# Performance work log

Measured on AMD Instinct MI355X. Metric: run time of the kernel, lower is better.

Reference implementation:

```python
import jax, jax.numpy as jnp
import numpy as np

N_EMBD = 1024
N_HEAD = 16
LATENT = 64
HEAD_DIM = N_EMBD // N_HEAD
B, T = 2, 2048
SCALE = 1.0 / np.sqrt(LATENT)


def setup_inputs() -> dict:
    key = jax.random.key(0)
    ks = jax.random.split(key, 10)
    s = lambda fan_in: 1.0 / np.sqrt(fan_in)
    return {
        "x": jax.random.normal(ks[0], (B, T, N_EMBD), dtype=jnp.float32),
        "Wq": jax.random.normal(ks[1], (N_EMBD, N_EMBD), dtype=jnp.float32) * s(N_EMBD),
        "bq": jnp.zeros((N_EMBD,), dtype=jnp.float32),
        "Wk": jax.random.normal(ks[2], (N_EMBD, N_HEAD * LATENT), dtype=jnp.float32) * s(N_EMBD),
        "bk": jnp.zeros((N_HEAD * LATENT,), dtype=jnp.float32),
        "Wv": jax.random.normal(ks[3], (N_EMBD, N_HEAD * LATENT), dtype=jnp.float32) * s(N_EMBD),
        "bv": jnp.zeros((N_HEAD * LATENT,), dtype=jnp.float32),
        "Wo": jax.random.normal(ks[4], (N_HEAD * LATENT, N_EMBD), dtype=jnp.float32) * s(N_HEAD * LATENT),
        "bo": jnp.zeros((N_EMBD,), dtype=jnp.float32),
        "Wc": jax.random.normal(ks[5], (HEAD_DIM, LATENT), dtype=jnp.float32) * s(HEAD_DIM),
    }


def reference(x, Wq, bq, Wk, bk, Wv, bv, Wo, bo, Wc):
    Bv, Tv, C = x.shape
    # projections
    q = (x @ Wq + bq).reshape(Bv, Tv, N_HEAD, HEAD_DIM)        # [B,T,H,Dh]
    k = (x @ Wk + bk).reshape(Bv, Tv, N_HEAD, LATENT)          # [B,T,H,L]
    v = (x @ Wv + bv).reshape(Bv, Tv, N_HEAD, LATENT)          # [B,T,H,L]
    # compress q into latent dim: [B,T,H,L]
    qc = jnp.einsum("bthd,dl->bthl", q, Wc)
    # attention scores [B,H,T,T]
    att = jnp.einsum("bthl,bshl->bhts", qc, k) * SCALE
    causal = jnp.tril(jnp.ones((Tv, Tv), dtype=bool))
    att = jnp.where(causal[None, None], att, -jnp.inf)
    att = jax.nn.softmax(att, axis=-1)
    y = jnp.einsum("bhts,bshl->bthl", att, v).reshape(Bv, Tv, N_HEAD * LATENT)
    return y @ Wo + bo
```

## Files before the change

### kernel.cpp

```cpp
#include <hip/hip_runtime.h>
#include <stdint.h>

#define TT 2048
#define BB 2
#define MROWS (BB*TT)
#define LSCALE 0.18033688011112043f

typedef unsigned short u16;
typedef __bf16 bf16x8 __attribute__((ext_vector_type(8)));
typedef float f32x4 __attribute__((ext_vector_type(4)));
typedef short s16x8 __attribute__((ext_vector_type(8)));
typedef unsigned short u16x4 __attribute__((ext_vector_type(4)));

#define GLOBAL_AS const __attribute__((address_space(1))) void*
#define LDS_AS __attribute__((address_space(3))) void*

__device__ __forceinline__ u16 f2b(float f){
  uint32_t u = __builtin_bit_cast(uint32_t, f);
  u = (u + 0x7FFFu + ((u >> 16) & 1u)) >> 16;
  return (u16)u;
}
__device__ __forceinline__ float b2f(u16 u){
  return __builtin_bit_cast(float, (uint32_t)u << 16);
}

__global__ void cvt_bf16(const float* __restrict__ in, u16* __restrict__ out, int n4){
  int i = blockIdx.x * 256 + threadIdx.x;
  if (i < n4){
    float4 v = ((const float4*)in)[i];
    u16x4 o; o.x = f2b(v.x); o.y = f2b(v.y); o.z = f2b(v.z); o.w = f2b(v.w);
    ((u16x4*)out)[i] = o;
  }
}

__global__ __launch_bounds__(256) void build_wqc(const float* __restrict__ Wq,
                                                 const float* __restrict__ Wc,
                                                 const float* __restrict__ bq,
                                                 float* __restrict__ Wqc,
                                                 float* __restrict__ bqc){
  __shared__ float wc[4096];
  const int t = threadIdx.x;
  #pragma unroll
  for (int i = 0; i < 16; ++i) wc[i * 256 + t] = Wc[i * 256 + t];
  __syncthreads();
  if (blockIdx.x == 256){
    #pragma unroll
    for (int i = 0; i < 4; ++i){
      int nn = t * 4 + i;
      int h = nn >> 6, lc = nn & 63;
      float acc = 0.f;
      #pragma unroll
      for (int dd = 0; dd < 64; ++dd) acc += bq[h * 64 + dd] * wc[dd * 64 + lc];
      bqc[nn] = acc;
    }
    return;
  }
  const int idx = blockIdx.x * 256 + t;
  const int d = idx >> 6;
  const int h = (idx >> 2) & 15;
  const int lq = idx & 3;
  float wqr[64];
  const float4* wq4 = (const float4*)(Wq + (size_t)d * 1024 + h * 64);
  #pragma unroll
  for (int i = 0; i < 16; ++i){
    float4 v = wq4[i];
    wqr[i * 4 + 0] = v.x; wqr[i * 4 + 1] = v.y; wqr[i * 4 + 2] = v.z; wqr[i * 4 + 3] = v.w;
  }
  float* outp = Wqc + (size_t)d * 1024 + h * 64 + lq * 16;
  #pragma unroll
  for (int j = 0; j < 16; ++j){
    int lc = lq * 16 + j;
    float acc = 0.f;
    #pragma unroll
    for (int dd = 0; dd < 64; ++dd) acc += wqr[dd] * wc[dd * 64 + lc];
    outp[j] = acc;
  }
}

__global__ void transpose_w4(const float* __restrict__ s0, const float* __restrict__ s1,
                             const float* __restrict__ s2, const float* __restrict__ s3,
                             u16* __restrict__ o0, u16* __restrict__ o1,
                             u16* __restrict__ o2, u16* __restrict__ o3){
  const int z = blockIdx.z;
  const float* in = (z == 0) ? s0 : (z == 1) ? s1 : (z == 2) ? s2 : s3;
  u16* out = (z == 0) ? o0 : (z == 1) ? o1 : (z == 2) ? o2 : o3;
  __shared__ float t[32][33];
  int tx = threadIdx.x & 31, ty = threadIdx.x >> 5;
  int c0 = blockIdx.x * 32, r0 = blockIdx.y * 32;
  #pragma unroll
  for (int i = 0; i < 32; i += 8)
    t[ty + i][tx] = in[(size_t)(r0 + ty + i) * 1024 + c0 + tx];
  __syncthreads();
  #pragma unroll
  for (int i = 0; i < 32; i += 8)
    out[(size_t)(c0 + ty + i) * 1024 + r0 + tx] = f2b(t[tx][ty + i]);
}

__global__ void transpose_v(const u16* __restrict__ vb, u16* __restrict__ vt){
  __shared__ u16 t[32][34];
  int tx = threadIdx.x & 31, ty = threadIdx.x >> 5;
  int s0 = blockIdx.x * 32, d0 = blockIdx.y * 32, bh = blockIdx.z;
  int b = bh >> 4, h = bh & 15;
  #pragma unroll
  for (int i = 0; i < 32; i += 8)
    t[ty + i][tx] = vb[(size_t)(b * TT + s0 + ty + i) * 1024 + h * 64 + d0 + tx];
  __syncthreads();
  #pragma unroll
  for (int i = 0; i < 32; i += 8)
    vt[((size_t)bh * 64 + d0 + ty + i) * TT + s0 + tx] = t[tx][ty + i];
}

__device__ __forceinline__ void gemm_tile(const u16* __restrict__ A, const u16* __restrict__ BT,
                                          int m0, int n0, int K, f32x4 (&acc)[4][4],
                                          u16* As, u16* Bs, int tid){
  const int wv = tid >> 6, l = tid & 63;
  const int aoff = ((wv >> 1) * 64 + (l & 15)) * 32 + ((l >> 4) << 3);
  const int boff = ((wv & 1) * 64 + (l & 15)) * 32 + ((l >> 4) << 3);
  const int ob0 = wv * 1024 + l * 16;
  for (int kt = 0; kt < K; kt += 32){
    __syncthreads();
    #pragma unroll
    for (int j = 0; j < 2; ++j){
      int ob = ob0 + j * 4096;
      int row = ob >> 6, col = (ob & 63) >> 1;
      __builtin_amdgcn_global_load_lds((GLOBAL_AS)(A + (size_t)(m0 + row) * 1024 + kt + col),
                                       (LDS_AS)(As + wv * 512 + j * 2048), 16, 0, 0);
      __builtin_amdgcn_global_load_lds((GLOBAL_AS)(BT + (size_t)(n0 + row) * 1024 + kt + col),
                                       (LDS_AS)(Bs + wv * 512 + j * 2048), 16, 0, 0);
    }
    __syncthreads();
    bf16x8 av[4], bw[4];
    #pragma unroll
    for (int m = 0; m < 4; ++m) av[m] = *(const bf16x8*)(As + aoff + m * 512);
    #pragma unroll
    for (int n = 0; n < 4; ++n) bw[n] = *(const bf16x8*)(Bs + boff + n * 512);
    #pragma unroll
    for (int m = 0; m < 4; ++m)
      #pragma unroll
      for (int n = 0; n < 4; ++n)
        acc[m][n] = __builtin_amdgcn_mfma_f32_16x16x32_bf16(av[m], bw[n], acc[m][n], 0, 0, 0);
  }
}

__global__ __launch_bounds__(256) void gemm_qkv(
    const u16* __restrict__ xb,
    const u16* __restrict__ W0T, const u16* __restrict__ W1T, const u16* __restrict__ W2T,
    const float* __restrict__ b0, const float* __restrict__ b1, const float* __restrict__ b2,
    u16* __restrict__ o0, u16* __restrict__ o1, u16* __restrict__ o2){
  __shared__ u16 As[4096], Bs[4096];
  const int z = blockIdx.z;
  const u16* BT = (z == 0) ? W0T : (z == 1) ? W1T : W2T;
  const float* bias = (z == 0) ? b0 : (z == 1) ? b1 : b2;
  u16* Out = (z == 0) ? o0 : (z == 1) ? o1 : o2;
  const float osc = (z == 0) ? LSCALE : 1.0f;
  const int n0 = blockIdx.x * 128, m0 = blockIdx.y * 128;
  const int tid = threadIdx.x, wv = tid >> 6, l = tid & 63;
  f32x4 acc[4][4] = {};
  gemm_tile(xb, BT, m0, n0, 1024, acc, As, Bs, tid);
  const int wr = wv >> 1, wc = wv & 1;
  #pragma unroll
  for (int n = 0; n < 4; ++n){
    int col = n0 + wc * 64 + n * 16 + (l & 15);
    float bb = bias[col];
    #pragma unroll
    for (int m = 0; m < 4; ++m){
      int r0 = m0 + wr * 64 + m * 16 + ((l >> 4) << 2);
      #pragma unroll
      for (int r = 0; r < 4; ++r)
        Out[(size_t)(r0 + r) * 1024 + col] = f2b((acc[m][n][r] + bb) * osc);
    }
  }
}

__global__ __launch_bounds__(256) void gemm_fp32out(
    const u16* __restrict__ A, const u16* __restrict__ BT,
    const float* __restrict__ bias, float* __restrict__ Out){
  __shared__ u16 As[4096], Bs[4096];
  const int n0 = blockIdx.x * 128, m0 = blockIdx.y * 128;
  const int tid = threadIdx.x, wv = tid >> 6, l = tid & 63;
  f32x4 acc[4][4] = {};
  gemm_tile(A, BT, m0, n0, 1024, acc, As, Bs, tid);
  const int wr = wv >> 1, wc = wv & 1;
  #pragma unroll
  for (int n = 0; n < 4; ++n){
    int col = n0 + wc * 64 + n * 16 + (l & 15);
    float bb = bias[col];
    #pragma unroll
    for (int m = 0; m < 4; ++m){
      int r0 = m0 + wr * 64 + m * 16 + ((l >> 4) << 2);
      #pragma unroll
      for (int r = 0; r < 4; ++r)
        Out[(size_t)(r0 + r) * 1024 + col] = acc[m][n][r] + bb;
    }
  }
}

__device__ const uint8_t gtab[48] = {
  31, 95, 30, 143,  94, 29, 93, 28, 142,  92, 27, 91, 26, 141,
  90, 25, 89, 24, 140,  88, 23, 87, 22, 139,  86, 21, 85, 20, 138,
  84, 19, 83, 18, 137,  82, 17, 81, 16, 136,  80, 135, 134, 133, 132,
  131, 130, 129, 128
};

__global__ __launch_bounds__(256) void attn(
    const u16* __restrict__ qcg, const u16* __restrict__ kg,
    const u16* __restrict__ vtg, u16* __restrict__ yg,
    u16* __restrict__ yp, float* __restrict__ mp, float* __restrict__ lp){
  __shared__ u16 Ks[4096], Vs[4096];
  __shared__ u16 Ps[4096];
  const int idx = blockIdx.x;
  const int g = idx >> 5, bh = idx & 31;
  const int gv_ = gtab[g];
  const int qt = gv_ & 31, piece = gv_ >> 6;
  const int hh = (qt + 2) >> 1;
  const int st0 = (piece == 1) ? hh : 0;
  const int st1 = (piece == 0) ? hh : qt + 1;
  const int pid = (piece == 2) ? -1 : ((31 - qt) * 32 + bh) * 2 + piece;
  const int b = bh >> 4, h = bh & 15;
  const int q0 = qt * 64;
  const int tid = threadIdx.x, wv = tid >> 6, l = tid & 63;
  const int c4 = l >> 4, q16 = l & 15;
  const size_t base = (size_t)b * TT * 1024 + h * 64;
  const u16* Q = qcg + base;
  const u16* K = kg + base;
  const u16* Vt = vtg + (size_t)bh * 64 * TT;

  const int sr = tid >> 3;
  const int sc = (tid & 7) ^ (sr & 7);
  const u16* gK = K + (size_t)sr * 1024 + sc * 8;
  const u16* gV = Vt + (size_t)sr * TT + sc * 8;

  bf16x8 qf[2];
  {
    int qr = q0 + wv * 16 + q16;
    #pragma unroll
    for (int ks = 0; ks < 2; ++ks)
      qf[ks] = *(const bf16x8*)(Q + (size_t)qr * 1024 + ks * 32 + (c4 << 3));
  }
  f32x4 yacc[4] = {};
  float mrow = -1e30f, srow = 0.f;

  uint32_t* const PsW = (uint32_t*)Ps + wv * 512 + q16 * 32;
  const int pm = (q16 & 7) << 2;

  u16* const kd = Ks + wv * 512;
  u16* const vd = Vs + wv * 512;

  for (int st = st0; st < st1; ++st){
    {
      const size_t o = (size_t)st * 64;
      __builtin_amdgcn_global_load_lds((GLOBAL_AS)(gK + o * 1024), (LDS_AS)kd, 16, 0, 0);
      __builtin_amdgcn_global_load_lds((GLOBAL_AS)(gK + (o + 32) * 1024), (LDS_AS)(kd + 2048), 16, 0, 0);
      __builtin_amdgcn_global_load_lds((GLOBAL_AS)(gV + o), (LDS_AS)vd, 16, 0, 0);
      __builtin_amdgcn_global_load_lds((GLOBAL_AS)(gV + o + 32 * TT), (LDS_AS)(vd + 2048), 16, 0, 0);
    }
    asm volatile("s_waitcnt vmcnt(0)" ::: "memory");
    __builtin_amdgcn_sched_barrier(0);
    __builtin_amdgcn_s_barrier();
    __builtin_amdgcn_sched_barrier(0);
    const int s0 = st * 64;
    f32x4 sf[4] = {};
    __builtin_amdgcn_s_setprio(1);
    #pragma unroll
    for (int ks = 0; ks < 2; ++ks)
      #pragma unroll
      for (int nf = 0; nf < 4; ++nf){
        int r = nf * 16 + q16, c = ks * 4 + c4;
        bf16x8 kf = *(const bf16x8*)(Ks + (r * 8 + (c ^ (r & 7))) * 8);
        sf[nf] = __builtin_amdgcn_mfma_f32_16x16x32_bf16(kf, qf[ks], sf[nf], 0, 0, 0);
      }
    __builtin_amdgcn_s_setprio(0);
    const int qa = q0 + wv * 16 + q16;
    float p[4][4];
    const bool domask = (st == qt);
    #pragma unroll
    for (int nf = 0; nf < 4; ++nf)
      #pragma unroll
      for (int r = 0; r < 4; ++r){
        float v_ = sf[nf][r];
        if (domask && (s0 + nf * 16 + c4 * 4 + r > qa)) v_ = -1e30f;
        p[nf][r] = v_;
      }
    float tmax = p[0][0];
    #pragma unroll
    for (int nf = 0; nf < 4; ++nf)
      #pragma unroll
      for (int r = 0; r < 4; ++r) tmax = fmaxf(tmax, p[nf][r]);
    tmax = fmaxf(tmax, __shfl_xor(tmax, 16));
    tmax = fmaxf(tmax, __shfl_xor(tmax, 32));
    if (__any(tmax > mrow + 8.0f)){
      float mnew = fmaxf(mrow, tmax);
      float resc = exp2f(mrow - mnew);
      srow *= resc;
      mrow = mnew;
      #pragma unroll
      for (int df = 0; df < 4; ++df)
        #pragma unroll
        for (int r = 0; r < 4; ++r) yacc[df][r] *= resc;
    }
    float tsum = 0.f;
    #pragma unroll
    for (int nf = 0; nf < 4; ++nf)
      #pragma unroll
      for (int r = 0; r < 4; ++r){ float e = exp2f(p[nf][r] - mrow); p[nf][r] = e; tsum += e; }
    tsum += __shfl_xor(tsum, 16);
    tsum += __shfl_xor(tsum, 32);
    srow += tsum;
    #pragma unroll
    for (int nf = 0; nf < 4; ++nf){
      uint32_t w0, w1;
      asm volatile("v_cvt_pk_bf16_f32 %0, %1, %2" : "=v"(w0) : "v"(p[nf][0]), "v"(p[nf][1]));
      asm volatile("v_cvt_pk_bf16_f32 %0, %1, %2" : "=v"(w1) : "v"(p[nf][2]), "v"(p[nf][3]));
      *(uint64_t*)(PsW + ((nf * 8 + c4 * 2) ^ pm)) = (uint64_t)w0 | ((uint64_t)w1 << 32);
    }
    asm volatile("s_waitcnt lgkmcnt(0)" ::: "memory");
    __builtin_amdgcn_sched_barrier(0);
    __builtin_amdgcn_s_setprio(1);
    #pragma unroll
    for (int ks2 = 0; ks2 < 2; ++ks2){
      bf16x8 pf = *(const bf16x8*)(PsW + ((ks2 * 16 + c4 * 4) ^ pm));
      #pragma unroll
      for (int df = 0; df < 4; ++df){
        int rd = df * 16 + q16, cd = ks2 * 4 + c4;
        bf16x8 vf = *(const bf16x8*)(Vs + (rd * 8 + (cd ^ (rd & 7))) * 8);
        yacc[df] = __builtin_amdgcn_mfma_f32_16x16x32_bf16(vf, pf, yacc[df], 0, 0, 0);
      }
    }
    __builtin_amdgcn_s_setprio(0);
    __builtin_amdgcn_s_barrier();
  }

  if (pid >= 0){
    const int qq = wv * 16 + q16;
    #pragma unroll
    for (int df = 0; df < 4; ++df){
      int d0 = df * 16 + c4 * 4;
      #pragma unroll
      for (int r = 0; r < 4; ++r)
        yp[(size_t)pid * 4096 + qq * 64 + d0 + r] = f2b(yacc[df][r]);
    }
    if (c4 == 0){
      mp[pid * 64 + qq] = mrow;
      lp[pid * 64 + qq] = srow;
    }
  } else {
    const float inv = 1.f / srow;
    const int qq = q0 + wv * 16 + q16;
    #pragma unroll
    for (int df = 0; df < 4; ++df){
      int d0 = df * 16 + c4 * 4;
      #pragma unroll
      for (int r = 0; r < 4; ++r)
        yg[(size_t)(b * TT + qq) * 1024 + h * 64 + d0 + r] = f2b(yacc[df][r] * inv);
    }
  }
}

__global__ __launch_bounds__(256) void attn_combine(
    const u16* __restrict__ yp, const float* __restrict__ mp, const float* __restrict__ lp,
    u16* __restrict__ yg){
  const int cid = blockIdx.x;
  const int qt = 31 - (cid >> 5), bh = cid & 31;
  const int pid0 = cid * 2;
  const int t = threadIdx.x;
  const int q = t >> 2, dc = (t & 3) * 16;
  float m1 = mp[pid0 * 64 + q], m2 = mp[(pid0 + 1) * 64 + q];
  float l1 = lp[pid0 * 64 + q], l2 = lp[(pid0 + 1) * 64 + q];
  float ms = fmaxf(m1, m2);
  float w1 = exp2f(m1 - ms), w2 = exp2f(m2 - ms);
  float inv = 1.f / (l1 * w1 + l2 * w2);
  w1 *= inv; w2 *= inv;
  const int b = bh >> 4, h = bh & 15;
  const s16x8* p1 = (const s16x8*)(yp + (size_t)pid0 * 4096 + q * 64 + dc);
  const s16x8* p2 = (const s16x8*)(yp + (size_t)(pid0 + 1) * 4096 + q * 64 + dc);
  u16* dst = yg + (size_t)(b * TT + qt * 64 + q) * 1024 + h * 64 + dc;
  #pragma unroll
  for (int j2 = 0; j2 < 2; ++j2){
    s16x8 a = p1[j2], c = p2[j2];
    s16x8 o;
    #pragma unroll
    for (int j = 0; j < 8; ++j)
      o[j] = (short)f2b(b2f((u16)a[j]) * w1 + b2f((u16)c[j]) * w2);
    *(s16x8*)(dst + j2 * 8) = o;
  }
}

extern "C" void kernel_launch(void* const* d_in, const int* in_sizes, int n_in,
                              void* d_out, int out_size, void* d_ws, size_t ws_size,
                              hipStream_t stream){
  (void)in_sizes; (void)n_in; (void)out_size; (void)ws_size;
  const float* x  = (const float*)d_in[0];
  const float* Wq = (const float*)d_in[1];
  const float* bq = (const float*)d_in[2];
  const float* Wk = (const float*)d_in[3];
  const float* bk = (const float*)d_in[4];
  const float* Wv = (const float*)d_in[5];
  const float* bv = (const float*)d_in[6];
  const float* Wo = (const float*)d_in[7];
  const float* bo = (const float*)d_in[8];
  const float* Wc = (const float*)d_in[9];
  float* out = (float*)d_out;

  char* wsb = (char*)d_ws;
  u16* xb    = (u16*)(wsb);
  u16* yb    = (u16*)(wsb);
  u16* qcb   = (u16*)(wsb + (8u  << 20));
  u16* kb    = (u16*)(wsb + (16u << 20));
  u16* vb    = (u16*)(wsb + (24u << 20));
  u16* yp    = (u16*)(wsb + (24u << 20));
  u16* vtb   = (u16*)(wsb + (33u << 20));
  float* Wqcf = (float*)(wsb + (33u << 20));
  float* mp  = (float*)(wsb + (41u << 20));
  float* lp  = (float*)(wsb + (41u << 20) + (1u<<19));
  u16* WqcT  = (u16*)(wsb + (42u << 20));
  u16* WkT   = (u16*)(wsb + (44u << 20));
  u16* WvT   = (u16*)(wsb + (46u << 20));
  u16* WoT   = (u16*)(wsb + (48u << 20));
  float* bqc  = (float*)(wsb + (50u << 20));

  cvt_bf16<<<4096, 256, 0, stream>>>(x, xb, MROWS * 1024 / 4);
  build_wqc<<<257, 256, 0, stream>>>(Wq, Wc, bq, Wqcf, bqc);
  transpose_w4<<<dim3(32, 32, 4), 256, 0, stream>>>(Wqcf, Wk, Wv, Wo, WqcT, WkT, WvT, WoT);
  gemm_qkv<<<dim3(8, 32, 3), 256, 0, stream>>>(xb, WqcT, WkT, WvT, bqc, bk, bv, qcb, kb, vb);
  transpose_v<<<dim3(64, 2, 32), 256, 0, stream>>>(vb, vtb);
  attn<<<dim3(1536), 256, 0, stream>>>(qcb, kb, vtb, yb, yp, mp, lp);
  attn_combine<<<dim3(512), 256, 0, stream>>>(yp, mp, lp, yb);
  gemm_fp32out<<<dim3(8, 32), 256, 0, stream>>>(yb, WoT, bo, out);
}
```

Baseline: 132.0 us.

## Fuse prep kernels, write V transposed from QKV GEMM, shrink output GEMM tile

Merges the x conversion, Wq·Wc fold, and weight transposes into one prep launch, so the fp32 Wqc intermediate no longer makes a round trip through memory. The QKV GEMM now writes V directly in the transposed layout attention needs, which removes the separate transpose_v kernel. The output projection GEMM uses 64-row tiles, giving 512 blocks for better CU coverage. The risks are that the V epilogue's strided 2-byte stores are poorly coalesced and that one heterogeneous prep kernel may balance its work unevenly across blocks.

```diff
diff --git a/kernel.cpp b/kernel.cpp
--- a/kernel.cpp
+++ b/kernel.cpp
@@ -24,90 +24,83 @@
   return __builtin_bit_cast(float, (uint32_t)u << 16);
 }
 
-__global__ void cvt_bf16(const float* __restrict__ in, u16* __restrict__ out, int n4){
-  int i = blockIdx.x * 256 + threadIdx.x;
-  if (i < n4){
-    float4 v = ((const float4*)in)[i];
+__global__ __launch_bounds__(256) void prep(
+    const float* __restrict__ x, const float* __restrict__ Wq,
+    const float* __restrict__ Wc, const float* __restrict__ bq,
+    const float* __restrict__ Wk, const float* __restrict__ Wv,
+    const float* __restrict__ Wo,
+    u16* __restrict__ xb, u16* __restrict__ WqcT, u16* __restrict__ WkT,
+    u16* __restrict__ WvT, u16* __restrict__ WoT, float* __restrict__ bqc){
+  const int i = blockIdx.x, t = threadIdx.x;
+  if (i < 4096){
+    int id = i * 256 + t;
+    float4 v = ((const float4*)x)[id];
     u16x4 o; o.x = f2b(v.x); o.y = f2b(v.y); o.z = f2b(v.z); o.w = f2b(v.w);
-    ((u16x4*)out)[i] = o;
-  }
-}
-
-__global__ __launch_bounds__(256) void build_wqc(const float* __restrict__ Wq,
-                                                 const float* __restrict__ Wc,
-                                                 const float* __restrict__ bq,
-                                                 float* __restrict__ Wqc,
-                                                 float* __restrict__ bqc){
+    ((u16x4*)xb)[id] = o;
+    return;
+  }
+  if (i < 7168){
+    int j = i - 4096;
+    int z = j >> 10, rem = j & 1023;
+    const float* in = (z == 0) ? Wk : (z == 1) ? Wv : Wo;
+    u16* out = (z == 0) ? WkT : (z == 1) ? WvT : WoT;
+    __shared__ float tl[32][33];
+    int tx = t & 31, ty = t >> 5;
+    int c0 = (rem & 31) * 32, r0 = (rem >> 5) * 32;
+    #pragma unroll
+    for (int k = 0; k < 32; k += 8)
+      tl[ty + k][tx] = in[(size_t)(r0 + ty + k) * 1024 + c0 + tx];
+    __syncthreads();
+    #pragma unroll
+    for (int k = 0; k < 32; k += 8)
+      out[(size_t)(c0 + ty + k) * 1024 + r0 + tx] = f2b(tl[tx][ty + k]);
+    return;
+  }
   __shared__ float wc[4096];
-  const int t = threadIdx.x;
   #pragma unroll
-  for (int i = 0; i < 16; ++i) wc[i * 256 + t] = Wc[i * 256 + t];
+  for (int k = 0; k < 16; ++k) wc[k * 256 + t] = Wc[k * 256 + t];
   __syncthreads();
-  if (blockIdx.x == 256){
-    #pragma unroll
-    for (int i = 0; i < 4; ++i){
-      int nn = t * 4 + i;
+  if (i == 7424){
+    #pragma unroll
+    for (int k = 0; k < 4; ++k){
+      int nn = t * 4 + k;
       int h = nn >> 6, lc = nn & 63;
-      float acc = 0.f;
-      #pragma unroll
-      for (int dd = 0; dd < 64; ++dd) acc += bq[h * 64 + dd] * wc[dd * 64 + lc];
-      bqc[nn] = acc;
+      float a = 0.f;
+      #pragma unroll
+      for (int dd = 0; dd < 64; ++dd) a += bq[h * 64 + dd] * wc[dd * 64 + lc];
+      bqc[nn] = a;
     }
     return;
   }
-  const int idx = blockIdx.x * 256 + t;
-  const int d = idx >> 6;
-  const int h = (idx >> 2) & 15;
-  const int lq = idx & 3;
-  float wqr[64];
-  const float4* wq4 = (const float4*)(Wq + (size_t)d * 1024 + h * 64);
-  #pragma unroll
-  for (int i = 0; i < 16; ++i){
-    float4 v = wq4[i];
-    wqr[i * 4 + 0] = v.x; wqr[i * 4 + 1] = v.y; wqr[i * 4 + 2] = v.z; wqr[i * 4 + 3] = v.w;
-  }
-  float* outp = Wqc + (size_t)d * 1024 + h * 64 + lq * 16;
-  #pragma unroll
-  for (int j = 0; j < 16; ++j){
-    int lc = lq * 16 + j;
-    float acc = 0.f;
-    #pragma unroll
-    for (int dd = 0; dd < 64; ++dd) acc += wqr[dd] * wc[dd * 64 + lc];
-    outp[j] = acc;
-  }
-}
-
-__global__ void transpose_w4(const float* __restrict__ s0, const float* __restrict__ s1,
-                             const float* __restrict__ s2, const float* __restrict__ s3,
-                             u16* __restrict__ o0, u16* __restrict__ o1,
-                             u16* __restrict__ o2, u16* __restrict__ o3){
-  const int z = blockIdx.z;
-  const float* in = (z == 0) ? s0 : (z == 1) ? s1 : (z == 2) ? s2 : s3;
-  u16* out = (z == 0) ? o0 : (z == 1) ? o1 : (z == 2) ? o2 : o3;
-  __shared__ float t[32][33];
-  int tx = threadIdx.x & 31, ty = threadIdx.x >> 5;
-  int c0 = blockIdx.x * 32, r0 = blockIdx.y * 32;
-  #pragma unroll
-  for (int i = 0; i < 32; i += 8)
-    t[ty + i][tx] = in[(size_t)(r0 + ty + i) * 1024 + c0 + tx];
+  __shared__ float tile[64][65];
+  const int j = i - 7168;
+  const int db = j >> 4, hb = j & 15;
+  {
+    int dl = t >> 2, lq = t & 3;
+    const float4* wq4 = (const float4*)(Wq + (size_t)(db * 64 + dl) * 1024 + hb * 64);
+    float wqr[64];
+    #pragma unroll
+    for (int k = 0; k < 16; ++k){
+      float4 v = wq4[k];
+      wqr[k * 4] = v.x; wqr[k * 4 + 1] = v.y; wqr[k * 4 + 2] = v.z; wqr[k * 4 + 3] = v.w;
+    }
+    #pragma unroll
+    for (int jj = 0; jj < 16; ++jj){
+      int lc = lq * 16 + jj;
+      float a = 0.f;
+      #pragma unroll
+      for (int dd = 0; dd < 64; ++dd) a += wqr[dd] * wc[dd * 64 + lc];
+      tile[dl][lc] = a;
+    }
+  }
   __syncthreads();
-  #pragma unroll
-  for (int i = 0; i < 32; i += 8)
-    out[(size_t)(c0 + ty + i) * 1024 + r0 + tx] = f2b(t[tx][ty + i]);
-}
-
-__global__ void transpose_v(const u16* __restrict__ vb, u16* __restrict__ vt){
-  __shared__ u16 t[32][34];
-  int tx = threadIdx.x & 31, ty = threadIdx.x >> 5;
-  int s0 = blockIdx.x * 32, d0 = blockIdx.y * 32, bh = blockIdx.z;
-  int b = bh >> 4, h = bh & 15;
-  #pragma unroll
-  for (int i = 0; i < 32; i += 8)
-    t[ty + i][tx] = vb[(size_t)(b * TT + s0 + ty + i) * 1024 + h * 64 + d0 + tx];
-  __syncthreads();
-  #pragma unroll
-  for (int i = 0; i < 32; i += 8)
-    vt[((size_t)bh * 64 + d0 + ty + i) * TT + s0 + tx] = t[tx][ty + i];
+  {
+    int nl = t >> 2, dq = t & 3;
+    u16* dst = WqcT + (size_t)(hb * 64 + nl) * 1024 + db * 64 + dq * 16;
+    #pragma unroll
+    for (int k = 0; k < 16; ++k)
+      dst[k] = f2b(tile[dq * 16 + k][nl]);
+  }
 }
 
 __device__ __forceinline__ void gemm_tile(const u16* __restrict__ A, const u16* __restrict__ BT,
@@ -146,18 +139,36 @@
     const u16* __restrict__ xb,
     const u16* __restrict__ W0T, const u16* __restrict__ W1T, const u16* __restrict__ W2T,
     const float* __restrict__ b0, const float* __restrict__ b1, const float* __restrict__ b2,
-    u16* __restrict__ o0, u16* __restrict__ o1, u16* __restrict__ o2){
+    u16* __restrict__ o0, u16* __restrict__ o1, u16* __restrict__ vt){
   __shared__ u16 As[4096], Bs[4096];
   const int z = blockIdx.z;
   const u16* BT = (z == 0) ? W0T : (z == 1) ? W1T : W2T;
   const float* bias = (z == 0) ? b0 : (z == 1) ? b1 : b2;
-  u16* Out = (z == 0) ? o0 : (z == 1) ? o1 : o2;
-  const float osc = (z == 0) ? LSCALE : 1.0f;
   const int n0 = blockIdx.x * 128, m0 = blockIdx.y * 128;
   const int tid = threadIdx.x, wv = tid >> 6, l = tid & 63;
   f32x4 acc[4][4] = {};
   gemm_tile(xb, BT, m0, n0, 1024, acc, As, Bs, tid);
   const int wr = wv >> 1, wc = wv & 1;
+  if (z == 2){
+    const int bb_ = m0 >> 11;
+    #pragma unroll
+    for (int n = 0; n < 4; ++n){
+      int col = n0 + wc * 64 + n * 16 + (l & 15);
+      float bb = bias[col];
+      int h = col >> 6, d = col & 63;
+      u16* dcol = vt + ((size_t)(bb_ * 16 + h) * 64 + d) * TT;
+      #pragma unroll
+      for (int m = 0; m < 4; ++m){
+        int s = (m0 & 2047) + wr * 64 + m * 16 + ((l >> 4) << 2);
+        #pragma unroll
+        for (int r = 0; r < 4; ++r)
+          dcol[s + r] = f2b(acc[m][n][r] + bb);
+      }
+    }
+    return;
+  }
+  u16* Out = (z == 0) ? o0 : o1;
+  const float osc = (z == 0) ? LSCALE : 1.0f;
   #pragma unroll
   for (int n = 0; n < 4; ++n){
     int col = n0 + wc * 64 + n * 16 + (l & 15);
@@ -172,22 +183,49 @@
   }
 }
 
-__global__ __launch_bounds__(256) void gemm_fp32out(
+__global__ __launch_bounds__(256) void gemm_o(
     const u16* __restrict__ A, const u16* __restrict__ BT,
     const float* __restrict__ bias, float* __restrict__ Out){
-  __shared__ u16 As[4096], Bs[4096];
-  const int n0 = blockIdx.x * 128, m0 = blockIdx.y * 128;
+  __shared__ u16 As[2048], Bs[4096];
+  const int n0 = blockIdx.x * 128, m0 = blockIdx.y * 64;
   const int tid = threadIdx.x, wv = tid >> 6, l = tid & 63;
-  f32x4 acc[4][4] = {};
-  gemm_tile(A, BT, m0, n0, 1024, acc, As, Bs, tid);
   const int wr = wv >> 1, wc = wv & 1;
+  const int aoff = (wr * 32 + (l & 15)) * 32 + ((l >> 4) << 3);
+  const int boff = (wc * 64 + (l & 15)) * 32 + ((l >> 4) << 3);
+  const int obA = wv * 1024 + l * 16;
+  const int rowA = obA >> 6, colA = (obA & 63) >> 1;
+  const int ob0 = wv * 1024 + l * 16;
+  f32x4 acc[2][4] = {};
+  for (int kt = 0; kt < 1024; kt += 32){
+    __syncthreads();
+    __builtin_amdgcn_global_load_lds((GLOBAL_AS)(A + (size_t)(m0 + rowA) * 1024 + kt + colA),
+                                     (LDS_AS)(As + wv * 512), 16, 0, 0);
+    #pragma unroll
+    for (int j = 0; j < 2; ++j){
+      int ob = ob0 + j * 4096;
+      int row = ob >> 6, col = (ob & 63) >> 1;
+      __builtin_amdgcn_global_load_lds((GLOBAL_AS)(BT + (size_t)(n0 + row) * 1024 + kt + col),
+                                       (LDS_AS)(Bs + wv * 512 + j * 2048), 16, 0, 0);
+    }
+    __syncthreads();
+    bf16x8 av[2], bw[4];
+    #pragma unroll
+    for (int m = 0; m < 2; ++m) av[m] = *(const bf16x8*)(As + aoff + m * 512);
+    #pragma unroll
+    for (int n = 0; n < 4; ++n) bw[n] = *(const bf16x8*)(Bs + boff + n * 512);
+    #pragma unroll
+    for (int m = 0; m < 2; ++m)
+      #pragma unroll
+      for (int n = 0; n < 4; ++n)
+        acc[m][n] = __builtin_amdgcn_mfma_f32_16x16x32_bf16(av[m], bw[n], acc[m][n], 0, 0, 0);
+  }
   #pragma unroll
   for (int n = 0; n < 4; ++n){
     int col = n0 + wc * 64 + n * 16 + (l & 15);
     float bb = bias[col];
     #pragma unroll
-    for (int m = 0; m < 4; ++m){
-      int r0 = m0 + wr * 64 + m * 16 + ((l >> 4) << 2);
+    for (int m = 0; m < 2; ++m){
+      int r0 = m0 + wr * 32 + m * 16 + ((l >> 4) << 2);
       #pragma unroll
       for (int r = 0; r < 4; ++r)
         Out[(size_t)(r0 + r) * 1024 + col] = acc[m][n][r] + bb;
@@ -406,24 +444,20 @@
   u16* yb    = (u16*)(wsb);
   u16* qcb   = (u16*)(wsb + (8u  << 20));
   u16* kb    = (u16*)(wsb + (16u << 20));
-  u16* vb    = (u16*)(wsb + (24u << 20));
   u16* yp    = (u16*)(wsb + (24u << 20));
   u16* vtb   = (u16*)(wsb + (33u << 20));
-  float* Wqcf = (float*)(wsb + (33u << 20));
   float* mp  = (float*)(wsb + (41u << 20));
-  float* lp  = (float*)(wsb + (41u << 20) + (1u<<19));
+  float* lp  = (float*)(wsb + (41u << 20) + (1u << 19));
   u16* WqcT  = (u16*)(wsb + (42u << 20));
   u16* WkT   = (u16*)(wsb + (44u << 20));
   u16* WvT   = (u16*)(wsb + (46u << 20));
   u16* WoT   = (u16*)(wsb + (48u << 20));
   float* bqc  = (float*)(wsb + (50u << 20));
 
-  cvt_bf16<<<4096, 256, 0, stream>>>(x, xb, MROWS * 1024 / 4);
-  build_wqc<<<257, 256, 0, stream>>>(Wq, Wc, bq, Wqcf, bqc);
-  transpose_w4<<<dim3(32, 32, 4), 256, 0, stream>>>(Wqcf, Wk, Wv, Wo, WqcT, WkT, WvT, WoT);
-  gemm_qkv<<<dim3(8, 32, 3), 256, 0, stream>>>(xb, WqcT, WkT, WvT, bqc, bk, bv, qcb, kb, vb);
-  transpose_v<<<dim3(64, 2, 32), 256, 0, stream>>>(vb, vtb);
+  prep<<<7425, 256, 0, stream>>>(x, Wq, Wc, bq, Wk, Wv, Wo,
+                                 xb, WqcT, WkT, WvT, WoT, bqc);
+  gemm_qkv<<<dim3(8, 32, 3), 256, 0, stream>>>(xb, WqcT, WkT, WvT, bqc, bk, bv, qcb, kb, vtb);
   attn<<<dim3(1536), 256, 0, stream>>>(qcb, kb, vtb, yb, yp, mp, lp);
   attn_combine<<<dim3(512), 256, 0, stream>>>(yp, mp, lp, yb);
-  gemm_fp32out<<<dim3(8, 32), 256, 0, stream>>>(yb, WoT, bo, out);
-}
+  gemm_o<<<dim3(8, 64), 256, 0, stream>>>(yb, WoT, bo, out);
+}
```

Result: slower. 141.1 us (+6.9%).
